# Kernel optimization log

Measured on AMD Instinct MI355X. Metric: run time of the kernel, lower is better.

Reference implementation:

```python
import jax, jax.numpy as jnp
import numpy as np

N_NODES = 50000
N_EDGES = 800000
BATCH = 128
D_IN = 768
D_H = 256
EPS_BN = 1e-5
EPS_COS = 1e-8


def setup_inputs() -> dict:
    key = jax.random.key(0)
    ks = jax.random.split(key, 16)
    s = 0.05
    return {
        "claim_embeddings": jax.random.normal(ks[0], (BATCH, D_IN), jnp.float32),
        "x": jax.random.normal(ks[1], (N_NODES, D_IN), jnp.float32),
        "edge_index": jax.random.randint(ks[2], (2, N_EDGES), 0, N_NODES, jnp.int32),
        "batch": jnp.sort(jax.random.randint(ks[3], (N_NODES,), 0, BATCH, jnp.int32)),
        "W1": jax.random.normal(ks[4], (D_IN, D_H), jnp.float32) * s,
        "a_src1": jax.random.normal(ks[5], (D_H,), jnp.float32) * s,
        "a_dst1": jax.random.normal(ks[6], (D_H,), jnp.float32) * s,
        "b1": jnp.zeros((D_H,), jnp.float32),
        "W2": jax.random.normal(ks[7], (D_H, D_H), jnp.float32) * s,
        "a_src2": jax.random.normal(ks[8], (D_H,), jnp.float32) * s,
        "a_dst2": jax.random.normal(ks[9], (D_H,), jnp.float32) * s,
        "b2": jnp.zeros((D_H,), jnp.float32),
        "bn_gamma": jnp.ones((D_H,), jnp.float32),
        "bn_beta": jnp.zeros((D_H,), jnp.float32),
        "Wc": jax.random.normal(ks[10], (D_H + D_IN, 1), jnp.float32) * s,
        "bc": jnp.zeros((1,), jnp.float32),
    }


def _gat_layer(h_in, src, dst, W, a_s, a_d, b, n_nodes):
    """PyG GATConv (heads=1, concat=True, self-loops already in src/dst)."""
    h = h_in @ W                                   # [N, D_H]
    alpha_s = h @ a_s                               # [N]
    alpha_d = h @ a_d                               # [N]
    e = jax.nn.leaky_relu(alpha_s[src] + alpha_d[dst], 0.2)  # [E+N]
    # numerically-stable softmax segmented by destination node
    e = e - jax.ops.segment_max(e, dst, num_segments=n_nodes)[dst]
    w = jnp.exp(e)
    w = w / jax.ops.segment_sum(w, dst, num_segments=n_nodes)[dst]
    out = jax.ops.segment_sum(h[src] * w[:, None], dst, num_segments=n_nodes)
    return out + b


def reference(claim_embeddings, x, edge_index, batch,
              W1, a_src1, a_dst1, b1, W2, a_src2, a_dst2, b2,
              bn_gamma, bn_beta, Wc, bc):
    n = x.shape[0]
    n_graphs = claim_embeddings.shape[0]
    # cosine-similarity relevance gating (torch eps semantics)
    ce = claim_embeddings[batch]                    # [N, D_IN]
    denom = jnp.maximum(jnp.linalg.norm(ce, axis=-1) * jnp.linalg.norm(x, axis=-1), EPS_COS)
    rel = jnp.sum(ce * x, axis=-1) / denom          # [N]
    h = x * rel[:, None]
    # add self-loops once (GATConv default add_self_loops=True)
    loops = jnp.arange(n, dtype=edge_index.dtype)
    src = jnp.concatenate([edge_index[0], loops])
    dst = jnp.concatenate([edge_index[1], loops])
    # layer 1 + batchnorm (batch stats) + relu
    h = _gat_layer(h, src, dst, W1, a_src1, a_dst1, b1, n)
    mean = jnp.mean(h, axis=0)
    var = jnp.mean(jnp.square(h - mean), axis=0)
    h = bn_gamma * (h - mean) * jax.lax.rsqrt(var + EPS_BN) + bn_beta
    h = jax.nn.relu(h)
    # layer 2 + relu
    h = _gat_layer(h, src, dst, W2, a_src2, a_dst2, b2, n)
    h = jax.nn.relu(h)
    # global mean pool per graph
    sums = jax.ops.segment_sum(h, batch, num_segments=n_graphs)
    counts = jax.ops.segment_sum(jnp.ones((n,), h.dtype), batch, num_segments=n_graphs)
    pooled = sums / jnp.maximum(counts, 1.0)[:, None]   # [B, D_H]
    combined = jnp.concatenate([pooled, claim_embeddings], axis=1)  # [B, D_H+D_IN]
    out = combined @ Wc + bc                        # [B, 1]
    return out.squeeze(-1)
```

## Files before the change

### kernel.cpp

```cpp
#include <hip/hip_runtime.h>
#include <hip/hip_bf16.h>

#define DIN 768
#define DH  256

typedef unsigned short ushort_t;
typedef unsigned char uchar_t;
typedef __attribute__((ext_vector_type(8))) short short8v;
typedef __attribute__((ext_vector_type(4))) float f32x4;
typedef __attribute__((ext_vector_type(2))) float f32x2;

__host__ __device__ inline int orig_col(int s) {
  int u = (s >> 2) & 31;
  return (s & ~127) | (((u >> 4) & 1) << 6) | ((s & 3) << 4) | (u & 15);
}

__device__ inline float wave_sum(float v) {
#pragma unroll
  for (int o = 32; o; o >>= 1) v += __shfl_xor(v, o);
  return v;
}
__device__ inline void wave_sum2(float& a, float& b) {
#pragma unroll
  for (int o = 32; o; o >>= 1) {
    a += __shfl_xor(a, o);
    b += __shfl_xor(b, o);
  }
}
__device__ inline float leaky(float v) { return v > 0.f ? v : 0.2f * v; }

__device__ inline ushort_t f2bf(float f) {
  union { float f; unsigned u; } v; v.f = f;
  unsigned r = v.u + 0x7FFFu + ((v.u >> 16) & 1u);
  return (ushort_t)(r >> 16);
}
__device__ inline float bf2f(ushort_t u) {
  union { unsigned u; float f; } t; t.u = ((unsigned)u) << 16; return t.f;
}

__device__ inline void unpack16f8(uint4 v, float* f) {
  f32x2 p;
  p = __builtin_amdgcn_cvt_pk_f32_fp8(v.x, false); f[0] = p[0]; f[1] = p[1];
  p = __builtin_amdgcn_cvt_pk_f32_fp8(v.x, true);  f[2] = p[0]; f[3] = p[1];
  p = __builtin_amdgcn_cvt_pk_f32_fp8(v.y, false); f[4] = p[0]; f[5] = p[1];
  p = __builtin_amdgcn_cvt_pk_f32_fp8(v.y, true);  f[6] = p[0]; f[7] = p[1];
  p = __builtin_amdgcn_cvt_pk_f32_fp8(v.z, false); f[8] = p[0]; f[9] = p[1];
  p = __builtin_amdgcn_cvt_pk_f32_fp8(v.z, true);  f[10] = p[0]; f[11] = p[1];
  p = __builtin_amdgcn_cvt_pk_f32_fp8(v.w, false); f[12] = p[0]; f[13] = p[1];
  p = __builtin_amdgcn_cvt_pk_f32_fp8(v.w, true);  f[14] = p[0]; f[15] = p[1];
}
__device__ inline uint4 pack8(const float* f) {
  uint4 o;
  o.x = (unsigned)f2bf(f[0]) | ((unsigned)f2bf(f[1]) << 16);
  o.y = (unsigned)f2bf(f[2]) | ((unsigned)f2bf(f[3]) << 16);
  o.z = (unsigned)f2bf(f[4]) | ((unsigned)f2bf(f[5]) << 16);
  o.w = (unsigned)f2bf(f[6]) | ((unsigned)f2bf(f[7]) << 16);
  return o;
}

__global__ __launch_bounds__(256) void rel_hist_kernel(
    const float* __restrict__ ce, const float* __restrict__ x,
    const int* __restrict__ batch, const float* __restrict__ cenorm,
    float* __restrict__ rel, int n,
    const int* __restrict__ edst, int E, int* __restrict__ cnt) {
  int node = blockIdx.x * 4 + (threadIdx.x >> 6);
  int lane = threadIdx.x & 63;
  if (node < n) {
    int g = batch[node];
    const float4* xr = (const float4*)(x + (size_t)node * DIN);
    const float4* cr = (const float4*)(ce + (size_t)g * DIN);
    float dxy = 0.f, dxx = 0.f;
#pragma unroll
    for (int i = 0; i < 3; i++) {
      float4 a = xr[lane + 64 * i];
      float4 b = cr[lane + 64 * i];
      dxy += a.x*b.x + a.y*b.y + a.z*b.z + a.w*b.w;
      dxx += a.x*a.x + a.y*a.y + a.z*a.z + a.w*a.w;
    }
    wave_sum2(dxy, dxx);
    if (lane == 0) {
      float denom = fmaxf(sqrtf(dxx) * cenorm[g], 1e-8f);
      rel[node] = dxy / denom;
    }
  }
  for (int e = blockIdx.x * blockDim.x + threadIdx.x; e < E;
       e += gridDim.x * blockDim.x)
    atomicAdd(&cnt[edst[e]], 1);
}

__global__ __launch_bounds__(256) void prep_kernel(
    const float* __restrict__ W1, const float* __restrict__ W2,
    const float* __restrict__ b1, const float* __restrict__ b2,
    const float* __restrict__ gamma, const float* __restrict__ beta,
    const float* __restrict__ Wc, const float* __restrict__ ce,
    ushort_t* __restrict__ Wt1, ushort_t* __restrict__ Wt2,
    float* __restrict__ pb1, float* __restrict__ pb2,
    float* __restrict__ pgamma, float* __restrict__ pbeta,
    float* __restrict__ pWc, float* __restrict__ cenorm, int B) {
  __shared__ float tile[64][65];
  int b = blockIdx.x;
  int t = threadIdx.x;
  int r4 = t >> 6;
  int c64 = t & 63;
  if (b < 48) {
    int k0 = (b % 12) * 64, c0 = (b / 12) * 64;
#pragma unroll
    for (int rr = 0; rr < 16; rr++) {
      int r = rr * 4 + r4;
      tile[r][c64] = W1[(size_t)(k0 + r) * 256 + c0 + c64];
    }
    __syncthreads();
#pragma unroll
    for (int rr = 0; rr < 16; rr++) {
      int cc = rr * 4 + r4;
      Wt1[(size_t)(c0 + cc) * DIN + k0 + c64] = f2bf(tile[c64][cc]);
    }
  } else if (b < 64) {
    int bb = b - 48;
    int k0 = (bb & 3) * 64, c0 = (bb >> 2) * 64;
#pragma unroll
    for (int rr = 0; rr < 16; rr++) {
      int r = rr * 4 + r4;
      tile[r][c64] = W2[(size_t)orig_col(k0 + r) * 256 + c0 + c64];
    }
    __syncthreads();
#pragma unroll
    for (int rr = 0; rr < 16; rr++) {
      int cc = rr * 4 + r4;
      Wt2[(size_t)(c0 + cc) * DH + k0 + c64] = f2bf(tile[c64][cc]);
    }
  } else if (b == 64) {
    int o = orig_col(t);
    pb1[t] = b1[o];
    pb2[t] = b2[o];
    pgamma[t] = gamma[o];
    pbeta[t] = beta[o];
    pWc[t] = Wc[o];
  } else {
    int lane = t & 63;
    for (int g = r4; g < B; g += 4) {
      const float4* cr = (const float4*)(ce + (size_t)g * DIN);
      float s = 0.f;
#pragma unroll
      for (int i = 0; i < 3; i++) {
        float4 v = cr[lane + 64 * i];
        s += v.x*v.x + v.y*v.y + v.z*v.z + v.w*v.w;
      }
      s = wave_sum(s);
      if (lane == 0) cenorm[g] = sqrtf(s);
    }
  }
}

__global__ __launch_bounds__(256) void scan1_kernel(const int* __restrict__ cnt,
                                                    int* __restrict__ row_off,
                                                    int* __restrict__ bsum, int n) {
  __shared__ int s[256];
  int t = threadIdx.x;
  int i = blockIdx.x * 256 + t;
  int v = (i < n) ? cnt[i] : 0;
  s[t] = v;
  __syncthreads();
  for (int off = 1; off < 256; off <<= 1) {
    int tmp = (t >= off) ? s[t - off] : 0;
    __syncthreads();
    s[t] += tmp;
    __syncthreads();
  }
  if (i < n) row_off[i] = s[t] - v;
  if (t == 255) bsum[blockIdx.x] = s[255];
}

__global__ __launch_bounds__(256) void scan2_kernel(const int* __restrict__ bsum,
                                                    int* __restrict__ boff, int nb,
                                                    int* __restrict__ row_off, int n) {
  __shared__ int s[256];
  int t = threadIdx.x;
  int v = (t < nb) ? bsum[t] : 0;
  s[t] = v;
  __syncthreads();
  for (int off = 1; off < 256; off <<= 1) {
    int tmp = (t >= off) ? s[t - off] : 0;
    __syncthreads();
    s[t] += tmp;
    __syncthreads();
  }
  if (t < nb) boff[t] = s[t] - v;
  if (t == nb - 1) row_off[n] = s[t];
}

__global__ __launch_bounds__(256) void scan3_kernel(int* __restrict__ row_off,
                                                    const int* __restrict__ boff, int n) {
  int i = blockIdx.x * 256 + threadIdx.x;
  if (i < n) row_off[i] += boff[blockIdx.x];
}

__global__ void fill_kernel(const int* __restrict__ src, const int* __restrict__ dst, int E,
                            const int* __restrict__ row_off, int* __restrict__ fill,
                            int* __restrict__ col_src) {
  for (int e = blockIdx.x * blockDim.x + threadIdx.x; e < E; e += gridDim.x * blockDim.x) {
    int d = dst[e];
    int slot = row_off[d] + atomicAdd(&fill[d], 1);
    col_src[slot] = src[e];
  }
}

__global__ __launch_bounds__(256) void gemm_mfma_f32A(
    const float* __restrict__ A, const ushort_t* __restrict__ Bt,
    uchar_t* __restrict__ C, const float* __restrict__ scale,
    const float* __restrict__ a_s, const float* __restrict__ a_d,
    float* __restrict__ alpha_s, float* __restrict__ alpha_d, int Mreal) {
  constexpr int K = DIN;
  __shared__ ushort_t ldsA[8192];
  __shared__ ushort_t ldsB[8192];
  const int tid = threadIdx.x;
  const int lane = tid & 63;
  const int wave = tid >> 6;

  int p = blockIdx.y * 2 + blockIdx.x;
  int total = 2 * gridDim.y;
  int cch = p >> 4;
  int v;
  if ((cch << 4) + 16 <= total) {
    int r = p & 15;
    v = (cch << 4) | ((r & 7) << 1) | (r >> 3);
  } else {
    v = p;
  }
  const int col0 = (v & 1) * 128;
  const int row0 = (v >> 1) * 128;

  const int wr = wave >> 1, wc = wave & 1;
  const int c16 = lane & 15, g4 = lane >> 4;

  const int st_row4 = tid >> 4;
  const int st_kq = tid & 15;
  const int stB_roff = lane >> 3;
  const int stB_gsrc = (lane & 7);

  f32x4 acc[4][4];
#pragma unroll
  for (int m = 0; m < 4; m++)
#pragma unroll
    for (int nn = 0; nn < 4; nn++)
#pragma unroll
      for (int j = 0; j < 4; j++) acc[m][nn][j] = 0.f;

  for (int k0 = 0; k0 < K; k0 += 64) {
#pragma unroll
    for (int ci = 0; ci < 4; ci++) {
      int j = wave * 4 + ci;
      int lrow = j * 8 + stB_roff;
      int ksrc = stB_gsrc ^ (lrow & 7);
      const ushort_t* gsrc = Bt + (size_t)(col0 + lrow) * K + k0 + ksrc * 8;
      __builtin_amdgcn_global_load_lds(
          (const __attribute__((address_space(1))) void*)gsrc,
          (__attribute__((address_space(3))) void*)&ldsB[j * 512], 16, 0, 0);
    }
#pragma unroll
    for (int i = 0; i < 8; i++) {
      int row = i * 16 + st_row4;
      int rg = row0 + row;
      rg = rg < Mreal ? rg : Mreal - 1;
      float4 a4 = *(const float4*)&A[(size_t)rg * K + k0 + st_kq * 4];
      unsigned u0, u1;
      asm("v_cvt_pk_bf16_f32 %0, %1, %2" : "=v"(u0) : "v"(a4.x), "v"(a4.y));
      asm("v_cvt_pk_bf16_f32 %0, %1, %2" : "=v"(u1) : "v"(a4.z), "v"(a4.w));
      int idx = row * 64 + ((st_kq >> 1) ^ (row & 7)) * 8 + (st_kq & 1) * 4;
      *(uint2*)&ldsA[idx] = make_uint2(u0, u1);
    }
    __syncthreads();
#pragma unroll
    for (int ks = 0; ks < 2; ks++) {
      int g = ks * 4 + g4;
      short8v a[4], b[4];
#pragma unroll
      for (int m = 0; m < 4; m++) {
        int ra = wr * 64 + m * 16 + c16;
        a[m] = *(const short8v*)&ldsA[ra * 64 + (g ^ (ra & 7)) * 8];
      }
#pragma unroll
      for (int nn = 0; nn < 4; nn++) {
        int rb = wc * 64 + nn * 16 + c16;
        b[nn] = *(const short8v*)&ldsB[rb * 64 + (g ^ (rb & 7)) * 8];
      }
#pragma unroll
      for (int m = 0; m < 4; m++)
#pragma unroll
        for (int nn = 0; nn < 4; nn++)
          acc[m][nn] = __builtin_amdgcn_mfma_f32_16x16x32_bf16(a[m], b[nn],
                                                               acc[m][nn], 0, 0, 0);
    }
    __syncthreads();
  }

  float asv[4], adv[4];
#pragma unroll
  for (int nn = 0; nn < 4; nn++) {
    int col = col0 + wc * 64 + nn * 16 + c16;
    asv[nn] = a_s[col];
    adv[nn] = a_d[col];
  }

  uint* Cw = (uint*)C;
#pragma unroll
  for (int m = 0; m < 4; m++) {
    int row_base = row0 + wr * 64 + m * 16 + g4 * 4;
#pragma unroll
    for (int j = 0; j < 4; j++) {
      int row = row_base + j;
      int rc = row < Mreal ? row : Mreal - 1;
      float s = scale ? scale[rc] : 1.0f;
      float vs[4];
      float ps = 0.f, pd = 0.f;
#pragma unroll
      for (int nn = 0; nn < 4; nn++) {
        float v2 = acc[m][nn][j] * s;
        vs[nn] = v2;
        ps = fmaf(v2, asv[nn], ps);
        pd = fmaf(v2, adv[nn], pd);
      }
#pragma unroll
      for (int o = 1; o < 16; o <<= 1) {
        ps += __shfl_xor(ps, o);
        pd += __shfl_xor(pd, o);
      }
      if (c16 == 0 && row < Mreal) {
        atomicAdd(&alpha_s[row], ps);
        atomicAdd(&alpha_d[row], pd);
      }
      if (row < Mreal) {
        unsigned w8 = __builtin_amdgcn_cvt_pk_fp8_f32(vs[0], vs[1], 0u, false);
        w8 = __builtin_amdgcn_cvt_pk_fp8_f32(vs[2], vs[3], w8, true);
        Cw[(size_t)row * 64 + (col0 >> 2) + wc * 16 + c16] = w8;
      }
    }
  }
}

template <int K>
__global__ __launch_bounds__(256) void gemm_mfma(
    const ushort_t* __restrict__ A, const ushort_t* __restrict__ Bt,
    uchar_t* __restrict__ C, const float* __restrict__ scale,
    const float* __restrict__ a_s, const float* __restrict__ a_d,
    float* __restrict__ alpha_s, float* __restrict__ alpha_d, int Mreal) {
  __shared__ ushort_t lds[16384];
  const int tid = threadIdx.x;
  const int lane = tid & 63;
  const int wave = tid >> 6;

  int p = blockIdx.y * 2 + blockIdx.x;
  int total = 2 * gridDim.y;
  int cch = p >> 4;
  int v;
  if ((cch << 4) + 16 <= total) {
    int r = p & 15;
    v = (cch << 4) | ((r & 7) << 1) | (r >> 3);
  } else {
    v = p;
  }
  const int col0 = (v & 1) * 128;
  const int row0 = (v >> 1) * 128;

  const int wr = wave >> 1, wc = wave & 1;
  const int c16 = lane & 15, g4 = lane >> 4;
  const int st_roff = lane >> 3;
  const int st_gsrc = (lane & 7) ^ st_roff;

  f32x4 acc[4][4];
#pragma unroll
  for (int m = 0; m < 4; m++)
#pragma unroll
    for (int nn = 0; nn < 4; nn++)
#pragma unroll
      for (int j = 0; j < 4; j++) acc[m][nn][j] = 0.f;

  for (int k0 = 0; k0 < K; k0 += 64) {
#pragma unroll
    for (int ci = 0; ci < 8; ci++) {
      int inst = wave * 8 + ci;
      int isB = inst >> 4;
      int idx = inst & 15;
      int lrow = idx * 8 + st_roff;
      const ushort_t* gsrc;
      if (isB == 0) {
        int rg = row0 + lrow;
        rg = rg < Mreal ? rg : Mreal - 1;
        gsrc = A + (size_t)rg * K + k0 + st_gsrc * 8;
      } else {
        gsrc = Bt + (size_t)(col0 + lrow) * K + k0 + st_gsrc * 8;
      }
      __builtin_amdgcn_global_load_lds(
          (const __attribute__((address_space(1))) void*)gsrc,
          (__attribute__((address_space(3))) void*)&lds[isB * 8192 + idx * 512],
          16, 0, 0);
    }
    __syncthreads();
#pragma unroll
    for (int ks = 0; ks < 2; ks++) {
      int g = ks * 4 + g4;
      short8v a[4], b[4];
#pragma unroll
      for (int m = 0; m < 4; m++) {
        int ra = wr * 64 + m * 16 + c16;
        a[m] = *(const short8v*)&lds[ra * 64 + (g ^ (ra & 7)) * 8];
      }
#pragma unroll
      for (int nn = 0; nn < 4; nn++) {
        int rb = wc * 64 + nn * 16 + c16;
        b[nn] = *(const short8v*)&lds[8192 + rb * 64 + (g ^ (rb & 7)) * 8];
      }
#pragma unroll
      for (int m = 0; m < 4; m++)
#pragma unroll
        for (int nn = 0; nn < 4; nn++)
          acc[m][nn] = __builtin_amdgcn_mfma_f32_16x16x32_bf16(a[m], b[nn],
                                                               acc[m][nn], 0, 0, 0);
    }
    __syncthreads();
  }

  float asv[4], adv[4];
#pragma unroll
  for (int nn = 0; nn < 4; nn++) {
    int col = col0 + wc * 64 + nn * 16 + c16;
    asv[nn] = a_s[col];
    adv[nn] = a_d[col];
  }

  uint* Cw = (uint*)C;
#pragma unroll
  for (int m = 0; m < 4; m++) {
    int row_base = row0 + wr * 64 + m * 16 + g4 * 4;
#pragma unroll
    for (int j = 0; j < 4; j++) {
      int row = row_base + j;
      int rc = row < Mreal ? row : Mreal - 1;
      float s = scale ? scale[rc] : 1.0f;
      float vs[4];
      float ps = 0.f, pd = 0.f;
#pragma unroll
      for (int nn = 0; nn < 4; nn++) {
        float v2 = acc[m][nn][j] * s;
        vs[nn] = v2;
        ps = fmaf(v2, asv[nn], ps);
        pd = fmaf(v2, adv[nn], pd);
      }
#pragma unroll
      for (int o = 1; o < 16; o <<= 1) {
        ps += __shfl_xor(ps, o);
        pd += __shfl_xor(pd, o);
      }
      if (c16 == 0 && row < Mreal) {
        atomicAdd(&alpha_s[row], ps);
        atomicAdd(&alpha_d[row], pd);
      }
      if (row < Mreal) {
        unsigned w8 = __builtin_amdgcn_cvt_pk_fp8_f32(vs[0], vs[1], 0u, false);
        w8 = __builtin_amdgcn_cvt_pk_fp8_f32(vs[2], vs[3], w8, true);
        Cw[(size_t)row * 64 + (col0 >> 2) + wc * 16 + c16] = w8;
      }
    }
  }
}

__global__ __launch_bounds__(256) void gat_agg(
    const uchar_t* __restrict__ h8, const float* __restrict__ as_,
    const float* __restrict__ ad_, const int* __restrict__ row_off,
    const int* __restrict__ col_src, const float* __restrict__ bias,
    ushort_t* __restrict__ outb, int n, int relu_out) {
  int node = blockIdx.x * 4 + (threadIdx.x >> 6);
  int lane = threadIdx.x & 63;
  if (node >= n) return;
  int lo = row_off[node], hi = row_off[node + 1];
  int deg = hi - lo;
  float adn = ad_[node];
  float w_self = __expf(leaky(as_[node] + adn));

  const int q = lane >> 4;
  const int l16 = lane & 15;
  const uchar_t* rowbase = h8 + (size_t)l16 * 16;

  float acc[16];
  float zacc = (lane == 0) ? w_self : 0.f;
  {
    uint4 v = *(const uint4*)(rowbase + (size_t)node * 256);
    float ws = (q == 0) ? w_self : 0.f;
    float f[16];
    unpack16f8(v, f);
#pragma unroll
    for (int i = 0; i < 16; i++) acc[i] = ws * f[i];
  }

  for (int base = 0; base < deg; base += 64) {
    int cnt = min(64, deg - base);
    int s = 0; float w = 0.f;
    if (lane < cnt) {
      s = col_src[lo + base + lane];
      w = __expf(leaky(as_[s] + adn));
    }
    zacc += w;
    int e = 0;
    for (; e + 8 <= cnt; e += 8) {
      int iA = e + q, iB = e + 4 + q;
      int sA = __shfl(s, iA);
      float wA = __shfl(w, iA);
      int sB = __shfl(s, iB);
      float wB = __shfl(w, iB);
      uint4 a0 = *(const uint4*)(rowbase + (size_t)sA * 256);
      uint4 b0 = *(const uint4*)(rowbase + (size_t)sB * 256);
      float f[16];
      unpack16f8(a0, f);
#pragma unroll
      for (int i = 0; i < 16; i++) acc[i] = fmaf(wA, f[i], acc[i]);
      unpack16f8(b0, f);
#pragma unroll
      for (int i = 0; i < 16; i++) acc[i] = fmaf(wB, f[i], acc[i]);
    }
    for (; e < cnt; e += 4) {
      int myE = e + q;
      int idx = myE < cnt ? myE : cnt - 1;
      int ss = __shfl(s, idx);
      float wv = __shfl(w, idx);
      float wgt = (myE < cnt) ? wv : 0.f;
      uint4 v = *(const uint4*)(rowbase + (size_t)ss * 256);
      float f[16];
      unpack16f8(v, f);
#pragma unroll
      for (int i = 0; i < 16; i++) acc[i] = fmaf(wgt, f[i], acc[i]);
    }
  }

  float z = wave_sum(zacc);
  float inv_z = 1.0f / z;

#pragma unroll
  for (int i = 0; i < 16; i++) {
    acc[i] += __shfl_xor(acc[i], 16);
    acc[i] += __shfl_xor(acc[i], 32);
  }

  if (q == 0) {
    float o[16];
#pragma unroll
    for (int i = 0; i < 16; i += 4) {
      float4 bb = *(const float4*)&bias[l16 * 16 + i];
      o[i]     = fmaf(acc[i],     inv_z, bb.x);
      o[i + 1] = fmaf(acc[i + 1], inv_z, bb.y);
      o[i + 2] = fmaf(acc[i + 2], inv_z, bb.z);
      o[i + 3] = fmaf(acc[i + 3], inv_z, bb.w);
    }
    if (relu_out) {
#pragma unroll
      for (int i = 0; i < 16; i++) o[i] = fmaxf(o[i], 0.f);
    }
    uint4* op = (uint4*)(outb + (size_t)node * 256 + l16 * 16);
    op[0] = pack8(o);
    op[1] = pack8(o + 8);
  }
}

__global__ __launch_bounds__(256) void bn_stats(const ushort_t* __restrict__ h, int n,
                                                float* __restrict__ bsum,
                                                float* __restrict__ bsq) {
  int c = threadIdx.x;
  int rows_per_block = (n + gridDim.x - 1) / gridDim.x;
  int r0 = blockIdx.x * rows_per_block;
  int r1 = min(r0 + rows_per_block, n);
  float sum = 0.f, sq = 0.f;
  for (int r = r0; r < r1; r++) {
    float v = bf2f(h[(size_t)r * 256 + c]);
    sum += v;
    sq = fmaf(v, v, sq);
  }
  atomicAdd(&bsum[c], sum);
  atomicAdd(&bsq[c], sq);
}

__global__ __launch_bounds__(256) void bn_apply(const ushort_t* __restrict__ h,
                                                const float* __restrict__ bsum,
                                                const float* __restrict__ bsq,
                                                const float* __restrict__ gamma,
                                                const float* __restrict__ beta,
                                                ushort_t* __restrict__ h2b, int n) {
  int total4 = n * 64;
  float inv_n = 1.0f / (float)n;
  for (int f = blockIdx.x * blockDim.x + threadIdx.x; f < total4;
       f += gridDim.x * blockDim.x) {
    int c4 = f & 63;
    uint2 hv = ((const uint2*)h)[f];
    float v0, v1, v2, v3;
    {
      union { unsigned u; float fl; } t;
      t.u = hv.x << 16;         v0 = t.fl;
      t.u = hv.x & 0xFFFF0000u; v1 = t.fl;
      t.u = hv.y << 16;         v2 = t.fl;
      t.u = hv.y & 0xFFFF0000u; v3 = t.fl;
    }
    float4 sm = ((const float4*)bsum)[c4];
    float4 sl = ((const float4*)bsq)[c4];
    float4 g = ((const float4*)gamma)[c4];
    float4 bb = ((const float4*)beta)[c4];
    float m, var;
    m = sm.x * inv_n; var = sl.x * inv_n - m * m;
    v0 = fmaxf(g.x * (v0 - m) * rsqrtf(var + 1e-5f) + bb.x, 0.f);
    m = sm.y * inv_n; var = sl.y * inv_n - m * m;
    v1 = fmaxf(g.y * (v1 - m) * rsqrtf(var + 1e-5f) + bb.y, 0.f);
    m = sm.z * inv_n; var = sl.z * inv_n - m * m;
    v2 = fmaxf(g.z * (v2 - m) * rsqrtf(var + 1e-5f) + bb.z, 0.f);
    m = sm.w * inv_n; var = sl.w * inv_n - m * m;
    v3 = fmaxf(g.w * (v3 - m) * rsqrtf(var + 1e-5f) + bb.w, 0.f);
    uint2 o;
    o.x = (unsigned)f2bf(v0) | ((unsigned)f2bf(v1) << 16);
    o.y = (unsigned)f2bf(v2) | ((unsigned)f2bf(v3) << 16);
    ((uint2*)h2b)[f] = o;
  }
}

__device__ inline int lower_bound_dev(const int* a, int n, int v) {
  int lo = 0, hi = n;
  while (lo < hi) {
    int mid = (lo + hi) >> 1;
    if (a[mid] < v) lo = mid + 1; else hi = mid;
  }
  return lo;
}

#define POOL_CHUNKS 16
__global__ __launch_bounds__(256) void pool_partial(const ushort_t* __restrict__ h,
                                                    const int* __restrict__ batch, int n,
                                                    float* __restrict__ psum) {
  int g = blockIdx.x / POOL_CHUNKS;
  int c = blockIdx.x % POOL_CHUNKS;
  int lo = lower_bound_dev(batch, n, g);
  int hi = lower_bound_dev(batch, n, g + 1);
  int len = hi - lo;
  int r0 = lo + (int)(((long long)len * c) / POOL_CHUNKS);
  int r1 = lo + (int)(((long long)len * (c + 1)) / POOL_CHUNKS);
  if (r1 <= r0) return;
  float sum = 0.f;
  for (int r = r0; r < r1; r++) sum += bf2f(h[(size_t)r * 256 + threadIdx.x]);
  atomicAdd(&psum[(size_t)g * 256 + threadIdx.x], sum);
}

__global__ __launch_bounds__(256) void final_kernel(const float* __restrict__ psum,
                                                    const int* __restrict__ batch, int n,
                                                    const float* __restrict__ ce,
                                                    const float* __restrict__ pWc,
                                                    const float* __restrict__ Wc,
                                                    const float* __restrict__ bc,
                                                    float* __restrict__ out, int B) {
  int g = blockIdx.x;
  int t = threadIdx.x;
  int lo = lower_bound_dev(batch, n, g);
  int hi = lower_bound_dev(batch, n, g + 1);
  float inv_cnt = 1.0f / fmaxf((float)(hi - lo), 1.0f);
  float p = 0.f;
  p = fmaf(psum[(size_t)g * 256 + t] * inv_cnt, pWc[t], p);
  p = fmaf(ce[(size_t)g * 768 + t],        Wc[256 + t], p);
  p = fmaf(ce[(size_t)g * 768 + 256 + t],  Wc[512 + t], p);
  p = fmaf(ce[(size_t)g * 768 + 512 + t],  Wc[768 + t], p);
  __shared__ float red[256];
  red[t] = p;
  __syncthreads();
  for (int s = 128; s; s >>= 1) {
    if (t < s) red[t] += red[t + s];
    __syncthreads();
  }
  if (t == 0) out[g] = red[0] + bc[0];
}

extern "C" void kernel_launch(void* const* d_in, const int* in_sizes, int n_in,
                              void* d_out, int out_size, void* d_ws, size_t ws_size,
                              hipStream_t stream) {
  const float* ce    = (const float*)d_in[0];
  const float* x     = (const float*)d_in[1];
  const int*   edge  = (const int*)d_in[2];
  const int*   batch = (const int*)d_in[3];
  const float* W1    = (const float*)d_in[4];
  const float* a_s1  = (const float*)d_in[5];
  const float* a_d1  = (const float*)d_in[6];
  const float* b1    = (const float*)d_in[7];
  const float* W2    = (const float*)d_in[8];
  const float* a_s2  = (const float*)d_in[9];
  const float* a_d2  = (const float*)d_in[10];
  const float* b2    = (const float*)d_in[11];
  const float* gamma = (const float*)d_in[12];
  const float* beta  = (const float*)d_in[13];
  const float* Wc    = (const float*)d_in[14];
  const float* bc    = (const float*)d_in[15];

  const int B = in_sizes[0] / DIN;
  const int n = in_sizes[1] / DIN;
  const int E = in_sizes[2] / 2;
  const int* esrc = edge;
  const int* edst = edge + E;

  char* w = (char*)d_ws;
  size_t off = 0;
  auto carve = [&](size_t bytes) -> void* {
    void* p = w + off;
    off = (off + bytes + 255) & ~(size_t)255;
    return p;
  };
  size_t hbytes  = (size_t)n * DH * 2;
  size_t h8bytes = (size_t)n * DH;
  ushort_t* h1b   = (ushort_t*)carve(hbytes);
  ushort_t* h2b   = (ushort_t*)carve(hbytes);
  ushort_t* buf_ob = (ushort_t*)carve(hbytes);
  uchar_t* buf_h8 = (uchar_t*)carve(h8bytes);
  int*   row_off = (int*)carve((size_t)(n + 1) * 4);
  int*   col_src = (int*)carve((size_t)E * 4);
  ushort_t* Wt1  = (ushort_t*)carve((size_t)DIN * DH * 2);
  ushort_t* Wt2  = (ushort_t*)carve((size_t)DH * DH * 2);
  float* pb1     = (float*)carve(DH * 4);
  float* pb2     = (float*)carve(DH * 4);
  float* pgamma  = (float*)carve(DH * 4);
  float* pbeta   = (float*)carve(DH * 4);
  float* pWc     = (float*)carve(DH * 4);
  float* cenorm  = (float*)carve((size_t)B * 4);
  float* rel     = (float*)carve((size_t)n * 4);
  int*   sc_bsum = (int*)carve(256 * 4);
  int*   sc_boff = (int*)carve(256 * 4);
  char* zero0 = (char*)carve((size_t)n * 4);
  int*   cnt     = (int*)zero0;
  int*   fill    = (int*)carve((size_t)n * 4);
  float* as1buf  = (float*)carve((size_t)n * 4);
  float* ad1buf  = (float*)carve((size_t)n * 4);
  float* as2buf  = (float*)carve((size_t)n * 4);
  float* ad2buf  = (float*)carve((size_t)n * 4);
  float* bn_sum  = (float*)carve(DH * 4);
  float* bn_sq   = (float*)carve(DH * 4);
  float* psum    = (float*)carve((size_t)B * DH * 4);
  size_t zero_bytes = (size_t)((char*)(psum + (size_t)B * DH) - zero0);

  hipMemsetAsync(zero0, 0, zero_bytes, stream);

  const int gN4 = (n + 3) / 4;
  const int Mb = (n + 127) / 128;
  const int nb = (n + 255) / 256;

  prep_kernel<<<66, 256, 0, stream>>>(W1, W2, b1, b2, gamma, beta, Wc, ce,
                                      Wt1, Wt2, pb1, pb2, pgamma, pbeta, pWc,
                                      cenorm, B);
  rel_hist_kernel<<<gN4, 256, 0, stream>>>(ce, x, batch, cenorm, rel, n,
                                           edst, E, cnt);
  scan1_kernel<<<nb, 256, 0, stream>>>(cnt, row_off, sc_bsum, n);
  scan2_kernel<<<1, 256, 0, stream>>>(sc_bsum, sc_boff, nb, row_off, n);
  scan3_kernel<<<nb, 256, 0, stream>>>(row_off, sc_boff, n);
  fill_kernel<<<1024, 256, 0, stream>>>(esrc, edst, E, row_off, fill, col_src);

  gemm_mfma_f32A<<<dim3(2, Mb), 256, 0, stream>>>(x, Wt1, buf_h8, rel, a_s1,
                                                  a_d1, as1buf, ad1buf, n);
  gat_agg<<<gN4, 256, 0, stream>>>(buf_h8, as1buf, ad1buf, row_off, col_src, pb1,
                                   h1b, n, 0);
  bn_stats<<<512, 256, 0, stream>>>(h1b, n, bn_sum, bn_sq);
  bn_apply<<<2048, 256, 0, stream>>>(h1b, bn_sum, bn_sq, pgamma, pbeta, h2b, n);

  gemm_mfma<DH><<<dim3(2, Mb), 256, 0, stream>>>(h2b, Wt2, buf_h8, nullptr, a_s2,
                                                 a_d2, as2buf, ad2buf, n);
  gat_agg<<<gN4, 256, 0, stream>>>(buf_h8, as2buf, ad2buf, row_off, col_src, pb2,
                                   buf_ob, n, 1);

  pool_partial<<<B * POOL_CHUNKS, 256, 0, stream>>>(buf_ob, batch, n, psum);
  final_kernel<<<B, 256, 0, stream>>>(psum, batch, n, ce, pWc, Wc, bc,
                                      (float*)d_out, B);
}
```

Baseline: 380.6 us.

## Widen layer-1 GEMM tile to full 256 output columns per block

The first GEMM now has each block compute a 128x256 tile covering all output columns, instead of two 128x128 blocks per row strip. The fp32 input rows of x are read from global memory and converted to bf16 once rather than twice. This halves the dominant A-matrix traffic and conversion work, and drops the block-swizzle logic. In exchange it doubles the accumulator registers and B tile LDS per block, which lowers occupancy and halves the grid size.

Measured after the change: 397.0 us (median of 2 runs). 1.04x slower.

```diff
diff --git a/kernel.cpp b/kernel.cpp
--- a/kernel.cpp
+++ b/kernel.cpp
@@ -205,30 +205,18 @@
   }
 }
 
-__global__ __launch_bounds__(256) void gemm_mfma_f32A(
+__global__ __launch_bounds__(256) void gemm1_k(
     const float* __restrict__ A, const ushort_t* __restrict__ Bt,
     uchar_t* __restrict__ C, const float* __restrict__ scale,
     const float* __restrict__ a_s, const float* __restrict__ a_d,
     float* __restrict__ alpha_s, float* __restrict__ alpha_d, int Mreal) {
   constexpr int K = DIN;
   __shared__ ushort_t ldsA[8192];
-  __shared__ ushort_t ldsB[8192];
+  __shared__ ushort_t ldsB[16384];
   const int tid = threadIdx.x;
   const int lane = tid & 63;
   const int wave = tid >> 6;
-
-  int p = blockIdx.y * 2 + blockIdx.x;
-  int total = 2 * gridDim.y;
-  int cch = p >> 4;
-  int v;
-  if ((cch << 4) + 16 <= total) {
-    int r = p & 15;
-    v = (cch << 4) | ((r & 7) << 1) | (r >> 3);
-  } else {
-    v = p;
-  }
-  const int col0 = (v & 1) * 128;
-  const int row0 = (v >> 1) * 128;
+  const int row0 = blockIdx.x * 128;
 
   const int wr = wave >> 1, wc = wave & 1;
   const int c16 = lane & 15, g4 = lane >> 4;
@@ -236,23 +224,23 @@
   const int st_row4 = tid >> 4;
   const int st_kq = tid & 15;
   const int stB_roff = lane >> 3;
-  const int stB_gsrc = (lane & 7);
-
-  f32x4 acc[4][4];
+  const int stB_gsrc = lane & 7;
+
+  f32x4 acc[4][8];
 #pragma unroll
   for (int m = 0; m < 4; m++)
 #pragma unroll
-    for (int nn = 0; nn < 4; nn++)
+    for (int nn = 0; nn < 8; nn++)
 #pragma unroll
       for (int j = 0; j < 4; j++) acc[m][nn][j] = 0.f;
 
   for (int k0 = 0; k0 < K; k0 += 64) {
 #pragma unroll
-    for (int ci = 0; ci < 4; ci++) {
-      int j = wave * 4 + ci;
+    for (int ci = 0; ci < 8; ci++) {
+      int j = wave * 8 + ci;
       int lrow = j * 8 + stB_roff;
       int ksrc = stB_gsrc ^ (lrow & 7);
-      const ushort_t* gsrc = Bt + (size_t)(col0 + lrow) * K + k0 + ksrc * 8;
+      const ushort_t* gsrc = Bt + (size_t)lrow * K + k0 + ksrc * 8;
       __builtin_amdgcn_global_load_lds(
           (const __attribute__((address_space(1))) void*)gsrc,
           (__attribute__((address_space(3))) void*)&ldsB[j * 512], 16, 0, 0);
@@ -273,31 +261,31 @@
 #pragma unroll
     for (int ks = 0; ks < 2; ks++) {
       int g = ks * 4 + g4;
-      short8v a[4], b[4];
+      short8v a[4], b[8];
 #pragma unroll
       for (int m = 0; m < 4; m++) {
         int ra = wr * 64 + m * 16 + c16;
         a[m] = *(const short8v*)&ldsA[ra * 64 + (g ^ (ra & 7)) * 8];
       }
 #pragma unroll
-      for (int nn = 0; nn < 4; nn++) {
-        int rb = wc * 64 + nn * 16 + c16;
+      for (int nn = 0; nn < 8; nn++) {
+        int rb = wc * 128 + nn * 16 + c16;
         b[nn] = *(const short8v*)&ldsB[rb * 64 + (g ^ (rb & 7)) * 8];
       }
 #pragma unroll
       for (int m = 0; m < 4; m++)
 #pragma unroll
-        for (int nn = 0; nn < 4; nn++)
+        for (int nn = 0; nn < 8; nn++)
           acc[m][nn] = __builtin_amdgcn_mfma_f32_16x16x32_bf16(a[m], b[nn],
                                                                acc[m][nn], 0, 0, 0);
     }
     __syncthreads();
   }
 
-  float asv[4], adv[4];
-#pragma unroll
-  for (int nn = 0; nn < 4; nn++) {
-    int col = col0 + wc * 64 + nn * 16 + c16;
+  float asv[8], adv[8];
+#pragma unroll
+  for (int nn = 0; nn < 8; nn++) {
+    int col = wc * 128 + nn * 16 + c16;
     asv[nn] = a_s[col];
     adv[nn] = a_d[col];
   }
@@ -311,10 +299,10 @@
       int row = row_base + j;
       int rc = row < Mreal ? row : Mreal - 1;
       float s = scale ? scale[rc] : 1.0f;
-      float vs[4];
+      float vs[8];
       float ps = 0.f, pd = 0.f;
 #pragma unroll
-      for (int nn = 0; nn < 4; nn++) {
+      for (int nn = 0; nn < 8; nn++) {
         float v2 = acc[m][nn][j] * s;
         vs[nn] = v2;
         ps = fmaf(v2, asv[nn], ps);
@@ -330,9 +318,14 @@
         atomicAdd(&alpha_d[row], pd);
       }
       if (row < Mreal) {
-        unsigned w8 = __builtin_amdgcn_cvt_pk_fp8_f32(vs[0], vs[1], 0u, false);
-        w8 = __builtin_amdgcn_cvt_pk_fp8_f32(vs[2], vs[3], w8, true);
-        Cw[(size_t)row * 64 + (col0 >> 2) + wc * 16 + c16] = w8;
+#pragma unroll
+        for (int hb = 0; hb < 2; hb++) {
+          unsigned w8 = __builtin_amdgcn_cvt_pk_fp8_f32(vs[4 * hb], vs[4 * hb + 1],
+                                                        0u, false);
+          w8 = __builtin_amdgcn_cvt_pk_fp8_f32(vs[4 * hb + 2], vs[4 * hb + 3],
+                                               w8, true);
+          Cw[(size_t)row * 64 + wc * 32 + hb * 16 + c16] = w8;
+        }
       }
     }
   }
@@ -750,8 +743,8 @@
   scan3_kernel<<<nb, 256, 0, stream>>>(row_off, sc_boff, n);
   fill_kernel<<<1024, 256, 0, stream>>>(esrc, edst, E, row_off, fill, col_src);
 
-  gemm_mfma_f32A<<<dim3(2, Mb), 256, 0, stream>>>(x, Wt1, buf_h8, rel, a_s1,
-                                                  a_d1, as1buf, ad1buf, n);
+  gemm1_k<<<Mb, 256, 0, stream>>>(x, Wt1, buf_h8, rel, a_s1, a_d1,
+                                  as1buf, ad1buf, n);
   gat_agg<<<gN4, 256, 0, stream>>>(buf_h8, as1buf, ad1buf, row_off, col_src, pb1,
                                    h1b, n, 0);
   bn_stats<<<512, 256, 0, stream>>>(h1b, n, bn_sum, bn_sq);
```
